# Optimization experiments

Measured on AMD Instinct MI355X. Metric: run time of the kernel, lower is better.

The kernel has to match this reference:

```python
import jax, jax.numpy as jnp
import numpy as np

D_Z, D_A = 128, 64
D = D_Z + D_A            # 192
H1, H2 = 512, 512
E, S = 16, 1
B, N = 64, 2048
LN_EPS = 1e-5


def mish(x):
    return x * jnp.tanh(jax.nn.softplus(x))


def layernorm(x, g, b):
    m = jnp.mean(x, axis=-1, keepdims=True)
    v = jnp.mean((x - m) ** 2, axis=-1, keepdims=True)
    return (x - m) * jax.lax.rsqrt(v + LN_EPS) * g + b


def setup_inputs() -> dict:
    key = jax.random.key(0)
    ks = jax.random.split(key, 12)
    inp = {
        "z": jax.random.normal(ks[0], (B, N, D_Z), jnp.float32),
        "a": jax.random.normal(ks[1], (B, N, D_A), jnp.float32),
        "phi": jax.random.normal(ks[2], (D, E, S), jnp.float32) / np.sqrt(D),
        # stacked per-expert params (vectorized over e)
        "W1": jax.random.normal(ks[3], (E, D, H1), jnp.float32) / np.sqrt(D),
        "b1": jnp.zeros((E, H1), jnp.float32),
        "g1": jnp.ones((E, H1), jnp.float32),
        "be1": jnp.zeros((E, H1), jnp.float32),
        "W2": jax.random.normal(ks[4], (E, H1, H2), jnp.float32) / np.sqrt(H1),
        "b2": jnp.zeros((E, H2), jnp.float32),
        "g2": jnp.ones((E, H2), jnp.float32),
        "be2": jnp.zeros((E, H2), jnp.float32),
        "W3": jax.random.normal(ks[5], (E, H2, D_Z), jnp.float32) / np.sqrt(H2),
        "b3": jnp.zeros((E, D_Z), jnp.float32),
    }
    return inp


def reference(z, a, phi, W1, b1, g1, be1, W2, b2, g2, be2, W3, b3):
    x = jnp.concatenate([z, a], axis=-1)                      # [B,N,D]
    weights = jnp.einsum('bnd,des->bnes', x, phi)             # [B,N,E,S]
    dispatch = jax.nn.softmax(weights, axis=1)                # over tokens N
    xin = jnp.einsum('bnes,bnd->besd', dispatch, x)           # [B,E,S,D]
    # batched per-expert MLP: NormedLinear -> NormedLinear -> Linear
    h = jnp.einsum('besd,edh->besh', xin, W1) + b1[None, :, None, :]
    h = mish(layernorm(h, g1[None, :, None, :], be1[None, :, None, :]))
    h = jnp.einsum('besh,ehk->besk', h, W2) + b2[None, :, None, :]
    h = mish(layernorm(h, g2[None, :, None, :], be2[None, :, None, :]))
    out_e = jnp.einsum('besk,ekz->besz', h, W3) + b3[None, :, None, :]
    expert_outputs = out_e.reshape(out_e.shape[0], E * S, D_Z)    # b (e s) z
    combine = jax.nn.softmax(weights.reshape(weights.shape[0], weights.shape[1], E * S), axis=-1)
    out = jnp.einsum('bnk,bkz->bnz', combine, expert_outputs)     # [B,N,d_z]
    return out
```

## Files before the change

kernel.cpp:

```cpp
#include <hip/hip_runtime.h>
#include <math.h>

#define BB 64
#define NN 2048
#define DZ 128
#define DA 64
#define DD 192
#define EE 16
#define HH 512
#define LN_EPS 1e-5f
#define NCH 32

typedef __attribute__((ext_vector_type(8))) short short8;
typedef __attribute__((ext_vector_type(4))) float f32x4;

__device__ __forceinline__ float mishf(float x) {
    float sp = (x > 20.f) ? x : log1pf(__expf(x));
    return x * tanhf(sp);
}

__device__ __forceinline__ unsigned short bf16_rne(float f) {
    unsigned u = __float_as_uint(f);
    return (unsigned short)((u + 0x7FFFu + ((u >> 16) & 1u)) >> 16);
}
__device__ __forceinline__ float bf16f(unsigned short h) {
    return __uint_as_float(((unsigned)h) << 16);
}

__global__ __launch_bounds__(256)
void k_phipack(const float* __restrict__ phi, unsigned short* __restrict__ ph,
               unsigned short* __restrict__ pl) {
    int idx = blockIdx.x * 256 + threadIdx.x;
    if (idx >= 6 * 64 * 8) return;
    int j = idx & 7, lane = (idx >> 3) & 63, kk = idx >> 9;
    int e = lane & 15, g = lane >> 4;
    int d = kk * 32 + g * 8 + j;
    float f = phi[d * EE + e];
    unsigned short h = bf16_rne(f);
    ph[idx] = h;
    pl[idx] = bf16_rne(f - bf16f(h));
}

__global__ __launch_bounds__(256)
void k_wxin(const float* __restrict__ z, const float* __restrict__ a,
            const unsigned short* __restrict__ php,
            const unsigned short* __restrict__ plp,
            float* __restrict__ w, float* __restrict__ pxin,
            float* __restrict__ pZ) {
    __shared__ unsigned int xhl[4 * 32 * 49];
    __shared__ float wexp[2][32 * 17];
    int ch2 = blockIdx.x, b = blockIdx.y;
    int t = threadIdx.x, wv = t >> 6, l = t & 63;
    int g = l >> 4, c = l & 15;

    auto phase0 = [&](int s) {
        long tok0 = (long)b * NN + (long)ch2 * 64 + s * 32;
        const float4* zp = (const float4*)(z + tok0 * DZ);
        const float4* ap = (const float4*)(a + tok0 * DA);
#pragma unroll
        for (int k = 0; k < 6; k++) {
            int f = t + k * 256;
            int tok = f / 48, q = f - tok * 48;
            float4 v = (q < 32) ? zp[tok * 32 + q] : ap[tok * 16 + (q - 32)];
            int reg = q / 12;
            int dq = q * 4 - reg * 48;
            unsigned* dst = &xhl[(reg * 32 + tok) * 49 + dq];
            const float* pv = &v.x;
#pragma unroll
            for (int i = 0; i < 4; i++) {
                unsigned short h = bf16_rne(pv[i]);
                unsigned short lo = bf16_rne(pv[i] - bf16f(h));
                dst[i] = ((unsigned)h << 16) | (unsigned)lo;
            }
        }
    };

    f32x4 acc0 = {0.f, 0.f, 0.f, 0.f};
    f32x4 acc1 = {0.f, 0.f, 0.f, 0.f};
    f32x4 acc2 = {0.f, 0.f, 0.f, 0.f};
    float zacc = 0.f;

    phase0(0);
    __syncthreads();

#pragma unroll
    for (int s = 0; s < 2; s++) {
        long tok0 = (long)b * NN + (long)ch2 * 64 + s * 32;

        short8 xh0, xl0, xh1, xl1, xh2, xl2;
#pragma unroll
        for (int j = 0; j < 8; j++) {
            int rowb = (wv * 32 + g * 8 + j) * 49;
            unsigned u0 = xhl[rowb + c];
            unsigned u1 = xhl[rowb + 16 + c];
            unsigned u2 = xhl[rowb + 32 + c];
            xh0[j] = (short)(u0 >> 16); xl0[j] = (short)(u0 & 0xffff);
            xh1[j] = (short)(u1 >> 16); xl1[j] = (short)(u1 & 0xffff);
            xh2[j] = (short)(u2 >> 16); xl2[j] = (short)(u2 & 0xffff);
        }

        if (wv < 2) {
            f32x4 accw = {0.f, 0.f, 0.f, 0.f};
#pragma unroll
            for (int kk = 0; kk < 6; kk++) {
                short8 bh = *(const short8*)(php + kk * 512 + l * 8);
                short8 bl = *(const short8*)(plp + kk * 512 + l * 8);
                int dbase = kk * 32 + g * 8;
                int reg = dbase / 48;
                int dq = dbase - reg * 48;
                int rowb = (reg * 32 + wv * 16 + c) * 49 + dq;
                short8 ah, al;
#pragma unroll
                for (int j = 0; j < 8; j++) {
                    unsigned u = xhl[rowb + j];
                    ah[j] = (short)(u >> 16);
                    al[j] = (short)(u & 0xffff);
                }
                accw = __builtin_amdgcn_mfma_f32_16x16x32_bf16(ah, bh, accw, 0, 0, 0);
                accw = __builtin_amdgcn_mfma_f32_16x16x32_bf16(al, bh, accw, 0, 0, 0);
                accw = __builtin_amdgcn_mfma_f32_16x16x32_bf16(ah, bl, accw, 0, 0, 0);
            }
#pragma unroll
            for (int r = 0; r < 4; r++) {
                long row_g = tok0 + wv * 16 + g * 4 + r;
                w[row_g * EE + c] = accw[r];
                wexp[s][(wv * 16 + g * 4 + r) * 17 + c] = __expf(accw[r]);
            }
        }
        __syncthreads();

        short8 ad;
#pragma unroll
        for (int j = 0; j < 8; j++) {
            float wf = wexp[s][(g * 8 + j) * 17 + c];
            ad[j] = (short)bf16_rne(wf);
            if (wv == 0) zacc += wf;
        }

        if (s == 0) phase0(1);

        acc0 = __builtin_amdgcn_mfma_f32_16x16x32_bf16(ad, xh0, acc0, 0, 0, 0);
        acc0 = __builtin_amdgcn_mfma_f32_16x16x32_bf16(ad, xl0, acc0, 0, 0, 0);
        acc1 = __builtin_amdgcn_mfma_f32_16x16x32_bf16(ad, xh1, acc1, 0, 0, 0);
        acc1 = __builtin_amdgcn_mfma_f32_16x16x32_bf16(ad, xl1, acc1, 0, 0, 0);
        acc2 = __builtin_amdgcn_mfma_f32_16x16x32_bf16(ad, xh2, acc2, 0, 0, 0);
        acc2 = __builtin_amdgcn_mfma_f32_16x16x32_bf16(ad, xl2, acc2, 0, 0, 0);

        if (s == 0) __syncthreads();
    }

    if (wv == 0) {
        zacc += __shfl_xor(zacc, 16);
        zacc += __shfl_xor(zacc, 32);
        if (l < 16) pZ[((long)ch2 * BB + b) * EE + c] = zacc;
    }

    float* pb = pxin + (long)ch2 * (EE * BB * DD) + (long)b * DD;
#pragma unroll
    for (int r = 0; r < 4; r++) {
        int e = g * 4 + r;
        float* pr = pb + (long)e * (BB * DD);
        pr[(wv * 3 + 0) * 16 + c] = acc0[r];
        pr[(wv * 3 + 1) * 16 + c] = acc1[r];
        pr[(wv * 3 + 2) * 16 + c] = acc2[r];
    }
}

__global__ __launch_bounds__(256)
void k_zred(const float* __restrict__ pZ, float* __restrict__ Zg) {
    int idx = blockIdx.x * 256 + threadIdx.x;
    if (idx >= BB * EE) return;
    float s = 0.f;
#pragma unroll 8
    for (int ch = 0; ch < NCH; ch++)
        s += pZ[(long)ch * (BB * EE) + idx];
    Zg[idx] = 1.f / s;
}

__global__ __launch_bounds__(256)
void k_xinred(const float* __restrict__ pxin, const float* __restrict__ Zg,
              float* __restrict__ xin) {
    long i = (long)blockIdx.x * 256 + threadIdx.x;
    int e = (int)(i / (BB * DD));
    int rem = (int)(i - (long)e * (BB * DD));
    int b = rem / DD;
    float s = 0.f;
#pragma unroll 8
    for (int ch = 0; ch < NCH; ch++)
        s += pxin[(long)ch * (EE * BB * DD) + i];
    xin[i] = s * Zg[b * EE + e];
}

__global__ __launch_bounds__(256)
void k_weights(const float* __restrict__ z, const float* __restrict__ a,
               const unsigned short* __restrict__ php,
               const unsigned short* __restrict__ plp,
               float* __restrict__ w) {
    int t = threadIdx.x;
    int wv = t >> 6, l = t & 63;
    long tokbase = ((long)blockIdx.x * 4 + wv) * 16;
    long tokA = tokbase + (l & 15);
    int g = l >> 4;

    short8 bh[6], bl[6], ah[6], al[6];
#pragma unroll
    for (int kk = 0; kk < 6; kk++) {
        bh[kk] = *(const short8*)(php + kk * 512 + l * 8);
        bl[kk] = *(const short8*)(plp + kk * 512 + l * 8);
    }
#pragma unroll
    for (int kk = 0; kk < 6; kk++) {
        int d0 = kk * 32 + g * 8;
        const float* src = (d0 < DZ) ? (z + tokA * DZ + d0)
                                     : (a + tokA * DA + (d0 - DZ));
        float4 v0 = ((const float4*)src)[0];
        float4 v1 = ((const float4*)src)[1];
        float f[8] = {v0.x, v0.y, v0.z, v0.w, v1.x, v1.y, v1.z, v1.w};
#pragma unroll
        for (int j = 0; j < 8; j++) {
            unsigned short h = bf16_rne(f[j]);
            ah[kk][j] = (short)h;
            al[kk][j] = (short)bf16_rne(f[j] - bf16f(h));
        }
    }
    f32x4 acc = {0.f, 0.f, 0.f, 0.f};
#pragma unroll
    for (int kk = 0; kk < 6; kk++)
        acc = __builtin_amdgcn_mfma_f32_16x16x32_bf16(ah[kk], bh[kk], acc, 0, 0, 0);
#pragma unroll
    for (int kk = 0; kk < 6; kk++)
        acc = __builtin_amdgcn_mfma_f32_16x16x32_bf16(al[kk], bh[kk], acc, 0, 0, 0);
#pragma unroll
    for (int kk = 0; kk < 6; kk++)
        acc = __builtin_amdgcn_mfma_f32_16x16x32_bf16(ah[kk], bl[kk], acc, 0, 0, 0);
    int e = l & 15;
#pragma unroll
    for (int r = 0; r < 4; r++) {
        long row = tokbase + g * 4 + r;
        w[row * EE + e] = acc[r];
    }
}

#define RSTR 17
__global__ __launch_bounds__(256)
void k_stats1(const float* __restrict__ w, float* __restrict__ lmax,
              float* __restrict__ lsum) {
    __shared__ float red[256 * RSTR];
    int b = blockIdx.y, c = blockIdx.x, t = threadIdx.x;
    const float* wb = w + ((long)b * NN + c * 512) * EE;
    float m[EE];
#pragma unroll
    for (int e = 0; e < EE; e++) m[e] = -1e30f;
    for (int k = 0; k < 2; k++) {
        const float4* row = (const float4*)(wb + ((long)(k * 256 + t)) * EE);
#pragma unroll
        for (int q = 0; q < 4; q++) {
            float4 v = row[q];
            m[q * 4 + 0] = fmaxf(m[q * 4 + 0], v.x);
            m[q * 4 + 1] = fmaxf(m[q * 4 + 1], v.y);
            m[q * 4 + 2] = fmaxf(m[q * 4 + 2], v.z);
            m[q * 4 + 3] = fmaxf(m[q * 4 + 3], v.w);
        }
    }
#pragma unroll
    for (int e = 0; e < EE; e++) red[t * RSTR + e] = m[e];
    __syncthreads();
    for (int s = 128; s > 0; s >>= 1) {
        if (t < s) {
#pragma unroll
            for (int e = 0; e < EE; e++)
                red[t * RSTR + e] = fmaxf(red[t * RSTR + e], red[(t + s) * RSTR + e]);
        }
        __syncthreads();
    }
    float mg[EE];
#pragma unroll
    for (int e = 0; e < EE; e++) mg[e] = red[e];
    __syncthreads();
    float s_[EE];
#pragma unroll
    for (int e = 0; e < EE; e++) s_[e] = 0.f;
    for (int k = 0; k < 2; k++) {
        const float4* row = (const float4*)(wb + ((long)(k * 256 + t)) * EE);
#pragma unroll
        for (int q = 0; q < 4; q++) {
            float4 v = row[q];
            s_[q * 4 + 0] += __expf(v.x - mg[q * 4 + 0]);
            s_[q * 4 + 1] += __expf(v.y - mg[q * 4 + 1]);
            s_[q * 4 + 2] += __expf(v.z - mg[q * 4 + 2]);
            s_[q * 4 + 3] += __expf(v.w - mg[q * 4 + 3]);
        }
    }
#pragma unroll
    for (int e = 0; e < EE; e++) red[t * RSTR + e] = s_[e];
    __syncthreads();
    for (int s = 128; s > 0; s >>= 1) {
        if (t < s) {
#pragma unroll
            for (int e = 0; e < EE; e++)
                red[t * RSTR + e] += red[(t + s) * RSTR + e];
        }
        __syncthreads();
    }
    if (t < EE) {
        lmax[((long)b * 4 + c) * EE + t] = mg[t];
        lsum[((long)b * 4 + c) * EE + t] = red[t];
    }
}

__global__ __launch_bounds__(256)
void k_stats2(const float* __restrict__ lmax, const float* __restrict__ lsum,
              float* __restrict__ gmax, float* __restrict__ grcp) {
    int idx = blockIdx.x * 256 + threadIdx.x;
    if (idx >= BB * EE) return;
    int b = idx >> 4, e = idx & 15;
    float gm = -1e30f;
#pragma unroll
    for (int c = 0; c < 4; c++)
        gm = fmaxf(gm, lmax[((long)b * 4 + c) * EE + e]);
    float Z = 0.f;
#pragma unroll
    for (int c = 0; c < 4; c++)
        Z += __expf(lmax[((long)b * 4 + c) * EE + e] - gm) * lsum[((long)b * 4 + c) * EE + e];
    gmax[idx] = gm;
    grcp[idx] = 1.f / Z;
}

__global__ __launch_bounds__(192)
void k_xin_scalar(const float* __restrict__ z, const float* __restrict__ a,
                  const float* __restrict__ w, const float* __restrict__ gmax,
                  const float* __restrict__ grcp, float* __restrict__ dst) {
    __shared__ float disp[128 * EE];
    int b = blockIdx.y, chunk = blockIdx.x, t = threadIdx.x;
    const float* wrow = w + ((long)b * NN + (long)chunk * 128) * EE;
    for (int i = t; i < 128 * EE; i += 192) {
        int e = i & 15;
        disp[i] = __expf(wrow[i] - gmax[b * EE + e]) * grcp[b * EE + e];
    }
    __syncthreads();
    const float* xp;
    int stride;
    if (t < DZ) { xp = z + ((long)b * NN + (long)chunk * 128) * DZ + t; stride = DZ; }
    else        { xp = a + ((long)b * NN + (long)chunk * 128) * DA + (t - DZ); stride = DA; }
    float acc[EE];
#pragma unroll
    for (int e = 0; e < EE; e++) acc[e] = 0.f;
    for (int n = 0; n < 128; n++) {
        float xv = xp[(long)n * stride];
        const float4* dp = (const float4*)(disp + n * EE);
#pragma unroll
        for (int q = 0; q < 4; q++) {
            float4 p = dp[q];
            acc[q * 4 + 0] += p.x * xv;
            acc[q * 4 + 1] += p.y * xv;
            acc[q * 4 + 2] += p.z * xv;
            acc[q * 4 + 3] += p.w * xv;
        }
    }
#pragma unroll
    for (int e = 0; e < EE; e++)
        atomicAdd(&dst[((long)e * BB + b) * DD + t], acc[e]);
}

template<int K, int OUT, int KSLICE, bool ADD_BIAS>
__global__ __launch_bounds__(256)
void k_gemm(const float* __restrict__ X, const float* __restrict__ W,
            const float* __restrict__ bias, float* __restrict__ Yp) {
    constexpr int SP = KSLICE + 4;
    constexpr int K4 = KSLICE / 4;
    __shared__ float xs[64 * SP];
    int cb = blockIdx.x, ks = blockIdx.y, e = blockIdx.z;
    int t = threadIdx.x;
    int k0 = ks * KSLICE;
    for (int i = t; i < 64 * K4; i += 256) {
        int r = i / K4, k4 = i % K4;
        *(float4*)&xs[r * SP + k4 * 4] =
            *(const float4*)(X + ((long)e * BB + r) * K + k0 + k4 * 4);
    }
    __syncthreads();
    int c = cb * 32 + (t & 7) * 4;
    int r0 = (t >> 3) * 2;
    const float* Wp = W + ((long)e * K + k0) * OUT + c;
    float acc0[4], acc1[4];
#pragma unroll
    for (int j = 0; j < 4; j++) {
        float bv = ADD_BIAS ? bias[(long)e * OUT + c + j] : 0.f;
        acc0[j] = bv;
        acc1[j] = bv;
    }
#pragma unroll 4
    for (int k4 = 0; k4 < K4; k4++) {
        float4 x0 = *(const float4*)&xs[r0 * SP + k4 * 4];
        float4 x1 = *(const float4*)&xs[(r0 + 1) * SP + k4 * 4];
        const float* xp0 = &x0.x;
        const float* xp1 = &x1.x;
#pragma unroll
        for (int j = 0; j < 4; j++) {
            float4 wv = *(const float4*)(Wp + (long)(k4 * 4 + j) * OUT);
            float xa = xp0[j], xb = xp1[j];
            acc0[0] += xa * wv.x; acc0[1] += xa * wv.y;
            acc0[2] += xa * wv.z; acc0[3] += xa * wv.w;
            acc1[0] += xb * wv.x; acc1[1] += xb * wv.y;
            acc1[2] += xb * wv.z; acc1[3] += xb * wv.w;
        }
    }
    float* yp = Yp + ((long)ks * (EE * BB) + (long)e * BB + r0) * OUT + c;
    *(float4*)yp         = make_float4(acc0[0], acc0[1], acc0[2], acc0[3]);
    *(float4*)(yp + OUT) = make_float4(acc1[0], acc1[1], acc1[2], acc1[3]);
}

template<int KS, bool HAS_BIAS>
__global__ __launch_bounds__(256)
void k_lnact(const float* __restrict__ Yp, const float* __restrict__ bias,
             const float* __restrict__ g, const float* __restrict__ be,
             float* __restrict__ Yo) {
    __shared__ float redS[4], redQ[4];
    int row = blockIdx.x, t = threadIdx.x;
    int e = row >> 6;
    float v[2];
#pragma unroll
    for (int j = 0; j < 2; j++) {
        int cj = t + j * 256;
        float s = HAS_BIAS ? bias[(long)e * HH + cj] : 0.f;
#pragma unroll
        for (int ks = 0; ks < KS; ks++)
            s += Yp[((long)ks * (EE * BB) + row) * HH + cj];
        v[j] = s;
    }
    float s = v[0] + v[1];
    float q = v[0] * v[0] + v[1] * v[1];
    for (int off = 32; off > 0; off >>= 1) {
        s += __shfl_xor(s, off);
        q += __shfl_xor(q, off);
    }
    int wave = t >> 6, lane = t & 63;
    if (lane == 0) { redS[wave] = s; redQ[wave] = q; }
    __syncthreads();
    float S = redS[0] + redS[1] + redS[2] + redS[3];
    float Q = redQ[0] + redQ[1] + redQ[2] + redQ[3];
    float mean = S * (1.f / HH);
    float var = Q * (1.f / HH) - mean * mean;
    float rstd = rsqrtf(var + LN_EPS);
#pragma unroll
    for (int j = 0; j < 2; j++) {
        int cj = t + j * 256;
        float gg = g[(long)e * HH + cj], bb = be[(long)e * HH + cj];
        Yo[(long)row * HH + cj] = mishf((v[j] - mean) * rstd * gg + bb);
    }
}

template<int KS>
__global__ __launch_bounds__(256)
void k_fin3(const float* __restrict__ p3, const float* __restrict__ b3,
            float* __restrict__ eout) {
    int t = threadIdx.x;
    int row = blockIdx.x * 2 + (t >> 7);
    int c = t & 127;
    int e = row >> 6, b = row & 63;
    float s = b3[(long)e * DZ + c];
#pragma unroll
    for (int ks = 0; ks < KS; ks++)
        s += p3[((long)ks * (EE * BB) + row) * DZ + c];
    eout[((long)b * EE + e) * DZ + c] = s;
}

__global__ __launch_bounds__(256)
void k_combine(const float* __restrict__ w, const float* __restrict__ eout,
               float* __restrict__ out) {
    __shared__ float comb[64][EE];
    __shared__ float eo[EE * DZ];
    int b = blockIdx.y, n0 = blockIdx.x * 64, t = threadIdx.x;
    for (int i = t; i < EE * DZ; i += 256) eo[i] = eout[(long)b * EE * DZ + i];
    int tok = t >> 2, sub = t & 3;
    const float4 wv = *(const float4*)(w + ((long)b * NN + n0 + tok) * EE + sub * 4);
    float mx = fmaxf(fmaxf(wv.x, wv.y), fmaxf(wv.z, wv.w));
    mx = fmaxf(mx, __shfl_xor(mx, 1, 4));
    mx = fmaxf(mx, __shfl_xor(mx, 2, 4));
    float e0 = __expf(wv.x - mx), e1 = __expf(wv.y - mx);
    float e2 = __expf(wv.z - mx), e3 = __expf(wv.w - mx);
    float s = e0 + e1 + e2 + e3;
    s += __shfl_xor(s, 1, 4);
    s += __shfl_xor(s, 2, 4);
    float rs = 1.f / s;
    comb[tok][sub * 4 + 0] = e0 * rs;
    comb[tok][sub * 4 + 1] = e1 * rs;
    comb[tok][sub * 4 + 2] = e2 * rs;
    comb[tok][sub * 4 + 3] = e3 * rs;
    __syncthreads();
    for (int i = t; i < 64 * DZ; i += 256) {
        int tk = i >> 7, c = i & 127;
        float acc = 0.f;
#pragma unroll
        for (int e = 0; e < EE; e++) acc += comb[tk][e] * eo[e * DZ + c];
        out[((long)b * NN + n0 + tk) * DZ + c] = acc;
    }
}

extern "C" void kernel_launch(void* const* d_in, const int* in_sizes, int n_in,
                              void* d_out, int out_size, void* d_ws, size_t ws_size,
                              hipStream_t stream) {
    const float* z   = (const float*)d_in[0];
    const float* a   = (const float*)d_in[1];
    const float* phi = (const float*)d_in[2];
    const float* W1  = (const float*)d_in[3];
    const float* b1  = (const float*)d_in[4];
    const float* g1  = (const float*)d_in[5];
    const float* be1 = (const float*)d_in[6];
    const float* W2  = (const float*)d_in[7];
    const float* b2  = (const float*)d_in[8];
    const float* g2  = (const float*)d_in[9];
    const float* be2 = (const float*)d_in[10];
    const float* W3  = (const float*)d_in[11];
    const float* b3  = (const float*)d_in[12];
    float* out = (float*)d_out;

    char* p = (char*)d_ws;
    float* w    = (float*)p; p += (size_t)BB * NN * EE * 4;
    float* gmax = (float*)p; p += (size_t)BB * EE * 4;
    float* grcp = (float*)p; p += (size_t)BB * EE * 4;
    float* lmax = (float*)p; p += (size_t)BB * 4 * EE * 4;
    float* lsum = (float*)p; p += (size_t)BB * 4 * EE * 4;
    float* xin  = (float*)p; p += (size_t)BB * EE * DD * 4;
    unsigned short* php = (unsigned short*)p; p += 6 * 64 * 8 * 2;
    unsigned short* plp = (unsigned short*)p; p += 6 * 64 * 8 * 2;
    float* pZ   = (float*)p; p += (size_t)NCH * BB * EE * 4;
    float* Zg   = (float*)p; p += (size_t)BB * EE * 4;
    char* region = p;
    float* pxin = (float*)region;
    float* part = (float*)region;
    float* h1   = (float*)(region + (size_t)4 * EE * BB * HH * 4);
    float* h2   = h1;
    float* eout = (float*)(region + (size_t)4 * EE * BB * HH * 4
                                  + (size_t)EE * BB * HH * 4);
    size_t region_off = (size_t)(region - (char*)d_ws);
    size_t need_full = region_off + (size_t)NCH * EE * BB * DD * 4;
    bool full = ws_size >= need_full;

    k_phipack<<<12, 256, 0, stream>>>(phi, php, plp);

    if (full) {
        k_wxin<<<dim3(NCH, BB), 256, 0, stream>>>(z, a, php, plp, w, pxin, pZ);
        k_zred<<<4, 256, 0, stream>>>(pZ, Zg);
        k_xinred<<<EE * BB * DD / 256, 256, 0, stream>>>(pxin, Zg, xin);
    } else {
        k_weights<<<BB * NN / 64, 256, 0, stream>>>(z, a, php, plp, w);
        k_stats1<<<dim3(4, BB), 256, 0, stream>>>(w, lmax, lsum);
        k_stats2<<<4, 256, 0, stream>>>(lmax, lsum, gmax, grcp);
        hipMemsetAsync(xin, 0, (size_t)BB * EE * DD * 4, stream);
        k_xin_scalar<<<dim3(NN / 128, BB), 192, 0, stream>>>(z, a, w, gmax, grcp, xin);
    }

    k_gemm<DD, HH, 96, false>
        <<<dim3(HH / 32, 2, EE), 256, 0, stream>>>(xin, W1, nullptr, part);
    k_lnact<2, true><<<EE * BB, 256, 0, stream>>>(part, b1, g1, be1, h1);

    k_gemm<HH, HH, 128, false>
        <<<dim3(HH / 32, 4, EE), 256, 0, stream>>>(h1, W2, nullptr, part);
    k_lnact<4, true><<<EE * BB, 256, 0, stream>>>(part, b2, g2, be2, h2);

    k_gemm<HH, DZ, 64, false>
        <<<dim3(DZ / 32, 8, EE), 256, 0, stream>>>(h2, W3, nullptr, part);
    k_fin3<8><<<EE * BB / 2, 256, 0, stream>>>(part, b3, eout);

    k_combine<<<dim3(NN / 64, BB), 256, 0, stream>>>(w, eout, out);
}
```

Measured before the change: 113.7 us.

## Restructure wxin to load x into registers directly and vectorize combine

```diff
diff --git a/kernel.cpp b/kernel.cpp
--- a/kernel.cpp
+++ b/kernel.cpp
@@ -47,122 +47,115 @@
             const unsigned short* __restrict__ plp,
             float* __restrict__ w, float* __restrict__ pxin,
             float* __restrict__ pZ) {
-    __shared__ unsigned int xhl[4 * 32 * 49];
-    __shared__ float wexp[2][32 * 17];
+    __shared__ unsigned int xp[32 * 196];
+    __shared__ float wexp[64 * 17];
     int ch2 = blockIdx.x, b = blockIdx.y;
     int t = threadIdx.x, wv = t >> 6, l = t & 63;
     int g = l >> 4, c = l & 15;
-
-    auto phase0 = [&](int s) {
-        long tok0 = (long)b * NN + (long)ch2 * 64 + s * 32;
-        const float4* zp = (const float4*)(z + tok0 * DZ);
-        const float4* ap = (const float4*)(a + tok0 * DA);
-#pragma unroll
-        for (int k = 0; k < 6; k++) {
-            int f = t + k * 256;
-            int tok = f / 48, q = f - tok * 48;
-            float4 v = (q < 32) ? zp[tok * 32 + q] : ap[tok * 16 + (q - 32)];
-            int reg = q / 12;
-            int dq = q * 4 - reg * 48;
-            unsigned* dst = &xhl[(reg * 32 + tok) * 49 + dq];
-            const float* pv = &v.x;
-#pragma unroll
-            for (int i = 0; i < 4; i++) {
-                unsigned short h = bf16_rne(pv[i]);
-                unsigned short lo = bf16_rne(pv[i] - bf16f(h));
-                dst[i] = ((unsigned)h << 16) | (unsigned)lo;
-            }
-        }
-    };
+    long tokA = (long)b * NN + (long)ch2 * 64 + wv * 16 + c;
+
+    f32x4 accw = {0.f, 0.f, 0.f, 0.f};
+#pragma unroll
+    for (int kk = 0; kk < 6; kk++) {
+        int d0 = kk * 32 + g * 8;
+        const float* src = (d0 < DZ) ? (z + tokA * DZ + d0)
+                                     : (a + tokA * DA + (d0 - DZ));
+        float4 v0 = ((const float4*)src)[0];
+        float4 v1 = ((const float4*)src)[1];
+        float f[8] = {v0.x, v0.y, v0.z, v0.w, v1.x, v1.y, v1.z, v1.w};
+        short8 ah, al;
+#pragma unroll
+        for (int j = 0; j < 8; j++) {
+            unsigned short h = bf16_rne(f[j]);
+            ah[j] = (short)h;
+            al[j] = (short)bf16_rne(f[j] - bf16f(h));
+        }
+        short8 bh = *(const short8*)(php + kk * 512 + l * 8);
+        short8 bl = *(const short8*)(plp + kk * 512 + l * 8);
+        accw = __builtin_amdgcn_mfma_f32_16x16x32_bf16(ah, bh, accw, 0, 0, 0);
+        accw = __builtin_amdgcn_mfma_f32_16x16x32_bf16(al, bh, accw, 0, 0, 0);
+        accw = __builtin_amdgcn_mfma_f32_16x16x32_bf16(ah, bl, accw, 0, 0, 0);
+
+        unsigned au[4], bu[4];
+#pragma unroll
+        for (int i = 0; i < 4; i++)
+            au[i] = ((unsigned)(unsigned short)ah[2 * i]) |
+                    (((unsigned)(unsigned short)ah[2 * i + 1]) << 16);
+#pragma unroll
+        for (int i = 0; i < 4; i++) bu[i] = (unsigned)__shfl_xor((int)au[i], 1);
+        unsigned o0, o1, o2, o3;
+        if ((c & 1) == 0) {
+            o0 = (au[0] & 0xffffu) | (bu[0] << 16);
+            o1 = (au[0] >> 16) | (bu[0] & 0xffff0000u);
+            o2 = (au[1] & 0xffffu) | (bu[1] << 16);
+            o3 = (au[1] >> 16) | (bu[1] & 0xffff0000u);
+        } else {
+            o0 = (bu[2] & 0xffffu) | (au[2] << 16);
+            o1 = (bu[2] >> 16) | (au[2] & 0xffff0000u);
+            o2 = (bu[3] & 0xffffu) | (au[3] << 16);
+            o3 = (bu[3] >> 16) | (au[3] & 0xffff0000u);
+        }
+        int tp = wv * 8 + (c >> 1);
+        uint4* dst = (uint4*)&xp[tp * 196 + d0 + (c & 1) * 4];
+        uint4 ov; ov.x = o0; ov.y = o1; ov.z = o2; ov.w = o3;
+        *dst = ov;
+    }
+#pragma unroll
+    for (int r = 0; r < 4; r++) {
+        long row = (long)b * NN + (long)ch2 * 64 + wv * 16 + g * 4 + r;
+        w[row * EE + c] = accw[r];
+        wexp[(wv * 16 + g * 4 + r) * 17 + c] = __expf(accw[r]);
+    }
+    __syncthreads();
 
     f32x4 acc0 = {0.f, 0.f, 0.f, 0.f};
     f32x4 acc1 = {0.f, 0.f, 0.f, 0.f};
     f32x4 acc2 = {0.f, 0.f, 0.f, 0.f};
     float zacc = 0.f;
-
-    phase0(0);
-    __syncthreads();
-
-#pragma unroll
-    for (int s = 0; s < 2; s++) {
-        long tok0 = (long)b * NN + (long)ch2 * 64 + s * 32;
-
-        short8 xh0, xl0, xh1, xl1, xh2, xl2;
+#pragma unroll
+    for (int ks = 0; ks < 2; ks++) {
+        short8 ad;
 #pragma unroll
         for (int j = 0; j < 8; j++) {
-            int rowb = (wv * 32 + g * 8 + j) * 49;
-            unsigned u0 = xhl[rowb + c];
-            unsigned u1 = xhl[rowb + 16 + c];
-            unsigned u2 = xhl[rowb + 32 + c];
-            xh0[j] = (short)(u0 >> 16); xl0[j] = (short)(u0 & 0xffff);
-            xh1[j] = (short)(u1 >> 16); xl1[j] = (short)(u1 & 0xffff);
-            xh2[j] = (short)(u2 >> 16); xl2[j] = (short)(u2 & 0xffff);
-        }
-
-        if (wv < 2) {
-            f32x4 accw = {0.f, 0.f, 0.f, 0.f};
-#pragma unroll
-            for (int kk = 0; kk < 6; kk++) {
-                short8 bh = *(const short8*)(php + kk * 512 + l * 8);
-                short8 bl = *(const short8*)(plp + kk * 512 + l * 8);
-                int dbase = kk * 32 + g * 8;
-                int reg = dbase / 48;
-                int dq = dbase - reg * 48;
-                int rowb = (reg * 32 + wv * 16 + c) * 49 + dq;
-                short8 ah, al;
-#pragma unroll
-                for (int j = 0; j < 8; j++) {
-                    unsigned u = xhl[rowb + j];
-                    ah[j] = (short)(u >> 16);
-                    al[j] = (short)(u & 0xffff);
-                }
-                accw = __builtin_amdgcn_mfma_f32_16x16x32_bf16(ah, bh, accw, 0, 0, 0);
-                accw = __builtin_amdgcn_mfma_f32_16x16x32_bf16(al, bh, accw, 0, 0, 0);
-                accw = __builtin_amdgcn_mfma_f32_16x16x32_bf16(ah, bl, accw, 0, 0, 0);
-            }
-#pragma unroll
-            for (int r = 0; r < 4; r++) {
-                long row_g = tok0 + wv * 16 + g * 4 + r;
-                w[row_g * EE + c] = accw[r];
-                wexp[s][(wv * 16 + g * 4 + r) * 17 + c] = __expf(accw[r]);
-            }
-        }
-        __syncthreads();
-
-        short8 ad;
-#pragma unroll
-        for (int j = 0; j < 8; j++) {
-            float wf = wexp[s][(g * 8 + j) * 17 + c];
+            float wf = wexp[(ks * 32 + g * 8 + j) * 17 + c];
             ad[j] = (short)bf16_rne(wf);
-            if (wv == 0) zacc += wf;
-        }
-
-        if (s == 0) phase0(1);
-
-        acc0 = __builtin_amdgcn_mfma_f32_16x16x32_bf16(ad, xh0, acc0, 0, 0, 0);
-        acc0 = __builtin_amdgcn_mfma_f32_16x16x32_bf16(ad, xl0, acc0, 0, 0, 0);
-        acc1 = __builtin_amdgcn_mfma_f32_16x16x32_bf16(ad, xh1, acc1, 0, 0, 0);
-        acc1 = __builtin_amdgcn_mfma_f32_16x16x32_bf16(ad, xl1, acc1, 0, 0, 0);
-        acc2 = __builtin_amdgcn_mfma_f32_16x16x32_bf16(ad, xh2, acc2, 0, 0, 0);
-        acc2 = __builtin_amdgcn_mfma_f32_16x16x32_bf16(ad, xl2, acc2, 0, 0, 0);
-
-        if (s == 0) __syncthreads();
-    }
-
-    if (wv == 0) {
-        zacc += __shfl_xor(zacc, 16);
-        zacc += __shfl_xor(zacc, 32);
-        if (l < 16) pZ[((long)ch2 * BB + b) * EE + c] = zacc;
-    }
+            zacc += wf;
+        }
+#pragma unroll
+        for (int dt = 0; dt < 3; dt++) {
+            int d = wv * 48 + dt * 16 + c;
+            int tpb = (ks * 16 + g * 4) * 196 + d;
+            unsigned u0 = xp[tpb];
+            unsigned u1 = xp[tpb + 196];
+            unsigned u2 = xp[tpb + 392];
+            unsigned u3 = xp[tpb + 588];
+            short8 xb;
+            xb[0] = (short)(u0 & 0xffffu); xb[1] = (short)(u0 >> 16);
+            xb[2] = (short)(u1 & 0xffffu); xb[3] = (short)(u1 >> 16);
+            xb[4] = (short)(u2 & 0xffffu); xb[5] = (short)(u2 >> 16);
+            xb[6] = (short)(u3 & 0xffffu); xb[7] = (short)(u3 >> 16);
+            if (dt == 0)
+                acc0 = __builtin_amdgcn_mfma_f32_16x16x32_bf16(ad, xb, acc0, 0, 0, 0);
+            else if (dt == 1)
+                acc1 = __builtin_amdgcn_mfma_f32_16x16x32_bf16(ad, xb, acc1, 0, 0, 0);
+            else
+                acc2 = __builtin_amdgcn_mfma_f32_16x16x32_bf16(ad, xb, acc2, 0, 0, 0);
+        }
+    }
+
+    zacc += __shfl_xor(zacc, 16);
+    zacc += __shfl_xor(zacc, 32);
+    if (wv == 0 && l < 16)
+        pZ[((long)ch2 * BB + b) * EE + c] = zacc;
 
     float* pb = pxin + (long)ch2 * (EE * BB * DD) + (long)b * DD;
 #pragma unroll
     for (int r = 0; r < 4; r++) {
         int e = g * 4 + r;
         float* pr = pb + (long)e * (BB * DD);
-        pr[(wv * 3 + 0) * 16 + c] = acc0[r];
-        pr[(wv * 3 + 1) * 16 + c] = acc1[r];
-        pr[(wv * 3 + 2) * 16 + c] = acc2[r];
+        pr[wv * 48 + c]      = acc0[r];
+        pr[wv * 48 + 16 + c] = acc1[r];
+        pr[wv * 48 + 32 + c] = acc2[r];
     }
 }
 
@@ -338,15 +331,15 @@
         disp[i] = __expf(wrow[i] - gmax[b * EE + e]) * grcp[b * EE + e];
     }
     __syncthreads();
-    const float* xp;
+    const float* xp_;
     int stride;
-    if (t < DZ) { xp = z + ((long)b * NN + (long)chunk * 128) * DZ + t; stride = DZ; }
-    else        { xp = a + ((long)b * NN + (long)chunk * 128) * DA + (t - DZ); stride = DA; }
+    if (t < DZ) { xp_ = z + ((long)b * NN + (long)chunk * 128) * DZ + t; stride = DZ; }
+    else        { xp_ = a + ((long)b * NN + (long)chunk * 128) * DA + (t - DZ); stride = DA; }
     float acc[EE];
 #pragma unroll
     for (int e = 0; e < EE; e++) acc[e] = 0.f;
     for (int n = 0; n < 128; n++) {
-        float xv = xp[(long)n * stride];
+        float xv = xp_[(long)n * stride];
         const float4* dp = (const float4*)(disp + n * EE);
 #pragma unroll
         for (int q = 0; q < 4; q++) {
@@ -470,7 +463,8 @@
     __shared__ float comb[64][EE];
     __shared__ float eo[EE * DZ];
     int b = blockIdx.y, n0 = blockIdx.x * 64, t = threadIdx.x;
-    for (int i = t; i < EE * DZ; i += 256) eo[i] = eout[(long)b * EE * DZ + i];
+    for (int i = t; i < EE * DZ / 4; i += 256)
+        ((float4*)eo)[i] = ((const float4*)(eout + (long)b * EE * DZ))[i];
     int tok = t >> 2, sub = t & 3;
     const float4 wv = *(const float4*)(w + ((long)b * NN + n0 + tok) * EE + sub * 4);
     float mx = fmaxf(fmaxf(wv.x, wv.y), fmaxf(wv.z, wv.w));
@@ -487,12 +481,18 @@
     comb[tok][sub * 4 + 2] = e2 * rs;
     comb[tok][sub * 4 + 3] = e3 * rs;
     __syncthreads();
-    for (int i = t; i < 64 * DZ; i += 256) {
-        int tk = i >> 7, c = i & 127;
-        float acc = 0.f;
-#pragma unroll
-        for (int e = 0; e < EE; e++) acc += comb[tk][e] * eo[e * DZ + c];
-        out[((long)b * NN + n0 + tk) * DZ + c] = acc;
+
+    for (int i = t; i < 64 * (DZ / 4); i += 256) {
+        int tk = i >> 5, c4 = (i & 31) * 4;
+        float ax = 0.f, ay = 0.f, az = 0.f, aw = 0.f;
+#pragma unroll
+        for (int e = 0; e < EE; e++) {
+            float cw = comb[tk][e];
+            float4 ev = *(const float4*)&eo[e * DZ + c4];
+            ax += cw * ev.x; ay += cw * ev.y;
+            az += cw * ev.z; aw += cw * ev.w;
+        }
+        *(float4*)&out[((long)b * NN + n0 + tk) * DZ + c4] = make_float4(ax, ay, az, aw);
     }
 }
 
```

Result: faster. 109.7 us (-3.5%).
